# Kernel tuning notes

Hardware: AMD Instinct MI355X
Metric: run time of the kernel (lower is better)

The kernel has to match this reference:

```python
import jax, jax.numpy as jnp
import numpy as np

BN_EPS = 1e-5
NUM_GRAPHS = 64


def setup_inputs() -> dict:
    key = jax.random.key(0)
    ks = jax.random.split(key, 16)
    N, E, C_in, H, L, G = 100000, 1600000, 32, 64, 4, NUM_GRAPHS
    x = jax.random.normal(ks[0], (N, C_in), dtype=jnp.float32)
    edge_index = jax.random.randint(ks[1], (2, E), 0, N, dtype=jnp.int64)
    batch = jnp.sort(jax.random.randint(ks[2], (N,), 0, G, dtype=jnp.int64))
    s_in = 1.0 / np.sqrt(C_in)
    s_h = 1.0 / np.sqrt(H)
    s_2h = 1.0 / np.sqrt(2 * H)
    Win = jax.random.uniform(ks[3], (C_in, H), jnp.float32, -s_in, s_in)
    bin_ = jax.random.uniform(ks[4], (H,), jnp.float32, -s_in, s_in)
    W1s = jax.random.uniform(ks[5], (L, H, 2 * H), jnp.float32, -s_h, s_h)
    b1s = jax.random.uniform(ks[6], (L, 2 * H), jnp.float32, -s_h, s_h)
    gammas = jnp.ones((L, 2 * H), jnp.float32)
    betas = jnp.zeros((L, 2 * H), jnp.float32)
    W2s = jax.random.uniform(ks[7], (L, 2 * H, H), jnp.float32, -s_2h, s_2h)
    b2s = jax.random.uniform(ks[8], (L, H), jnp.float32, -s_2h, s_2h)
    epss = jnp.zeros((L,), jnp.float32)
    Wout = jax.random.uniform(ks[9], (H, 1), jnp.float32, -s_h, s_h)
    bout = jax.random.uniform(ks[10], (1,), jnp.float32, -s_h, s_h)
    return {"x": x, "edge_index": edge_index, "batch": batch, "Win": Win,
            "bin_": bin_, "W1s": W1s, "b1s": b1s, "gammas": gammas,
            "betas": betas, "W2s": W2s, "b2s": b2s, "epss": epss,
            "Wout": Wout, "bout": bout}


def _gin_layer(x, src, dst, W1, b1, gamma, beta, W2, b2, eps, n_nodes):
    # message: relu of source node features; aggregate: scatter-add at target
    agg = jax.ops.segment_sum(jax.nn.relu(x[src]), dst, num_segments=n_nodes)
    h = (1.0 + eps) * x + agg
    h = h @ W1 + b1
    mu = jnp.mean(h, axis=0)
    var = jnp.mean(jnp.square(h - mu), axis=0)  # biased, as in BatchNorm1d
    h = (h - mu) * jax.lax.rsqrt(var + BN_EPS) * gamma + beta
    h = jax.nn.relu(h)
    return h @ W2 + b2


def reference(x, edge_index, batch, Win, bin_, W1s, b1s, gammas, betas,
              W2s, b2s, epss, Wout, bout):
    N = x.shape[0]
    src, dst = edge_index[0], edge_index[1]
    x = x @ Win + bin_
    for l in range(W1s.shape[0]):
        x = x + _gin_layer(x, src, dst, W1s[l], b1s[l], gammas[l], betas[l],
                           W2s[l], b2s[l], epss[l], N)
    pooled = jax.ops.segment_sum(x, batch, num_segments=NUM_GRAPHS)  # [G, H]
    out = pooled @ Wout + bout
    return out.reshape(-1)
```

## Files before the change

kernel.cpp:

```cpp
#include <hip/hip_runtime.h>
#include <hip/hip_fp16.h>

#define H 64
#define CIN 32
#define TWOH 128
#define NGRAPH 64

#define BSH 7
#define BNODE 128
#define NBLK_PART 256
#define BCAP 32
#define MAXNB 2048
#define OCAP 65536

typedef unsigned short bfraw;
typedef _Float16 v8h __attribute__((ext_vector_type(8)));
typedef unsigned short v8u __attribute__((ext_vector_type(8)));
typedef float v4f __attribute__((ext_vector_type(4)));

union h8cast { v8u u; v8h h; uint4 q; };

__device__ __forceinline__ bfraw f2h(float f) {
    return __half_as_ushort(__float2half(f));
}
__device__ __forceinline__ float h2f(bfraw u) {
    return __half2float(__ushort_as_half(u));
}
__device__ __forceinline__ __half2 u2h2(unsigned u) {
    union { unsigned u; __half2 h; } c; c.u = u; return c.h;
}
__device__ __forceinline__ void f2h2(float f, _Float16& hi, _Float16& lo) {
    hi = (_Float16)f;
    lo = (_Float16)(f - (float)hi);
}

extern "C" __global__ void __launch_bounds__(256) k_input_gemm(
    const float* __restrict__ x, const float* __restrict__ Win,
    const float* __restrict__ bin, float* __restrict__ x0,
    bfraw* __restrict__ xh, int N)
{
    const int lane = threadIdx.x & 63;
    const int row = lane & 15;
    const int kg  = lane >> 4;
    v8h bhi[4], blo[4];
    #pragma unroll
    for (int ct = 0; ct < 4; ++ct) {
        v8h bh, bl;
        #pragma unroll
        for (int i = 0; i < 8; ++i) {
            const float w = Win[(kg * 8 + i) * H + ct * 16 + row];
            _Float16 h, l; f2h2(w, h, l);
            bh[i] = h; bl[i] = l;
        }
        bhi[ct] = bh; blo[ct] = bl;
    }
    float bcol[4];
    #pragma unroll
    for (int ct = 0; ct < 4; ++ct) bcol[ct] = bin[ct * 16 + row];

    const int wpb = blockDim.x >> 6;
    const int wid = blockIdx.x * wpb + (threadIdx.x >> 6);
    const int wstride = gridDim.x * wpb;
    const int tiles = (N + 15) >> 4;
    for (int t = wid; t < tiles; t += wstride) {
        const int tb = t << 4;
        int nA = tb + row; if (nA >= N) nA = N - 1;
        v8h a;
        #pragma unroll
        for (int i = 0; i < 8; ++i)
            a[i] = (_Float16)x[(size_t)nA * CIN + kg * 8 + i];
        v4f c[4];
        #pragma unroll
        for (int ct = 0; ct < 4; ++ct) {
            v4f cc = (v4f){0.f, 0.f, 0.f, 0.f};
            cc = __builtin_amdgcn_mfma_f32_16x16x32_f16(a, bhi[ct], cc, 0, 0, 0);
            cc = __builtin_amdgcn_mfma_f32_16x16x32_f16(a, blo[ct], cc, 0, 0, 0);
            c[ct] = cc;
        }
        #pragma unroll
        for (int ct = 0; ct < 4; ++ct) {
            #pragma unroll
            for (int r = 0; r < 4; ++r) {
                const int node = tb + kg * 4 + r;
                if (node < N) {
                    const float v = c[ct][r] + bcol[ct];
                    const size_t idx = (size_t)node * H + ct * 16 + row;
                    x0[idx] = v;
                    xh[idx] = f2h(fmaxf(v, 0.f));
                }
            }
        }
    }
}

extern "C" __global__ void k_cvtw(const float* __restrict__ W1s,
    const float* __restrict__ W2s, bfraw* __restrict__ W1hi,
    bfraw* __restrict__ W1lo, bfraw* __restrict__ W2hi,
    bfraw* __restrict__ W2lo, int total)
{
    int i = blockIdx.x * blockDim.x + threadIdx.x;
    const int st = gridDim.x * blockDim.x;
    for (; i < total; i += st) {
        {
            const float w = W1s[i];
            const bfraw hb = f2h(w);
            W1hi[i] = hb;
            W1lo[i] = f2h(w - h2f(hb));
        }
        {
            const float w = W2s[i];
            const bfraw hb = f2h(w);
            W2hi[i] = hb;
            W2lo[i] = f2h(w - h2f(hb));
        }
    }
}

__device__ __forceinline__ void bput(int s, int d, unsigned* __restrict__ lcnt,
    unsigned* __restrict__ myTmp, unsigned* __restrict__ deg,
    int* __restrict__ oflow, unsigned* __restrict__ ocnt)
{
    const int b = d >> BSH;
    const unsigned pos = atomicAdd(&lcnt[b], 1u);
    if (pos < BCAP) {
        myTmp[b * BCAP + pos] = (unsigned)s | ((unsigned)(d & (BNODE - 1)) << 20);
    } else {
        const unsigned o = atomicAdd(ocnt, 1u);
        if (o < OCAP) {
            oflow[2 * o] = s; oflow[2 * o + 1] = d;
            atomicAdd(&deg[d], 1u);
        }
    }
}

extern "C" __global__ void __launch_bounds__(256) k_bucket(
    const int* __restrict__ src, const int* __restrict__ dst,
    unsigned* __restrict__ bcnt, unsigned* __restrict__ btmp,
    unsigned* __restrict__ deg, int* __restrict__ oflow,
    unsigned* __restrict__ ocnt, int E, int NBck)
{
    __shared__ unsigned lcnt[MAXNB];
    for (int i = threadIdx.x; i < NBck; i += blockDim.x) lcnt[i] = 0u;
    __syncthreads();
    unsigned* __restrict__ myTmp = btmp + (size_t)blockIdx.x * NBck * BCAP;
    const int tid0 = blockIdx.x * blockDim.x + threadIdx.x;
    const int st = gridDim.x * blockDim.x;
    const int E4 = E >> 2;
    const int4* s4 = (const int4*)src;
    const int4* d4 = (const int4*)dst;
    for (int j = tid0; j < E4; j += st) {
        const int4 sv = s4[j];
        const int4 dv = d4[j];
        bput(sv.x, dv.x, lcnt, myTmp, deg, oflow, ocnt);
        bput(sv.y, dv.y, lcnt, myTmp, deg, oflow, ocnt);
        bput(sv.z, dv.z, lcnt, myTmp, deg, oflow, ocnt);
        bput(sv.w, dv.w, lcnt, myTmp, deg, oflow, ocnt);
    }
    for (int j = (E4 << 2) + tid0; j < E; j += st)
        bput(src[j], dst[j], lcnt, myTmp, deg, oflow, ocnt);
    __syncthreads();
    unsigned* __restrict__ myCnt = bcnt + (size_t)blockIdx.x * NBck;
    for (int i = threadIdx.x; i < NBck; i += blockDim.x) {
        const unsigned c = lcnt[i];
        myCnt[i] = (c < BCAP) ? c : BCAP;
    }
}

extern "C" __global__ void __launch_bounds__(256) k_bhist(
    const unsigned* __restrict__ bcnt, const unsigned* __restrict__ btmp,
    unsigned* __restrict__ deg, int N, int NBck)
{
    __shared__ unsigned hist[BNODE];
    const int b = blockIdx.x;
    for (int i = threadIdx.x; i < BNODE; i += blockDim.x) hist[i] = 0u;
    __syncthreads();
    for (int blk = threadIdx.x; blk < NBLK_PART; blk += blockDim.x) {
        const unsigned cnt = bcnt[(size_t)blk * NBck + b];
        const unsigned* p = btmp + ((size_t)blk * NBck + b) * BCAP;
        for (unsigned j = 0; j < cnt; ++j)
            atomicAdd(&hist[p[j] >> 20], 1u);
    }
    __syncthreads();
    const int base = b << BSH;
    for (int i = threadIdx.x; i < BNODE; i += blockDim.x)
        if (base + i < N) {
            const unsigned h = hist[i];
            if (h) atomicAdd(&deg[base + i], h);
        }
}

extern "C" __global__ void k_scan1(const unsigned* __restrict__ deg,
    unsigned* __restrict__ indptr, unsigned* __restrict__ bsum, int N)
{
    __shared__ unsigned s[256];
    const int tid = threadIdx.x;
    const int base = blockIdx.x * 1024 + tid * 4;
    unsigned d[4];
    #pragma unroll
    for (int j = 0; j < 4; ++j)
        d[j] = (base + j < N) ? ((deg[base + j] + 7u) & ~7u) : 0u;
    unsigned t = d[0] + d[1] + d[2] + d[3];
    s[tid] = t;
    __syncthreads();
    for (int o = 1; o < 256; o <<= 1) {
        unsigned v = (tid >= o) ? s[tid - o] : 0u;
        __syncthreads();
        s[tid] += v;
        __syncthreads();
    }
    unsigned run = (tid == 0) ? 0u : s[tid - 1];
    if (tid == 255) bsum[blockIdx.x] = s[255];
    #pragma unroll
    for (int j = 0; j < 4; ++j) {
        if (base + j < N) indptr[base + j] = run;
        run += d[j];
    }
}

extern "C" __global__ void k_scan2(unsigned* bsum, int nb,
    unsigned* __restrict__ indptr, int N,
    const float* __restrict__ bout, float* __restrict__ out)
{
    if (threadIdx.x < NGRAPH) out[threadIdx.x] = bout[0];
    if (threadIdx.x == 0) {
        unsigned run = 0;
        for (int i = 0; i < nb; ++i) { unsigned v = bsum[i]; bsum[i] = run; run += v; }
        indptr[N] = run;
    }
}

extern "C" __global__ void k_scan3(unsigned* __restrict__ indptr,
    const unsigned* __restrict__ bsum, unsigned* __restrict__ cursor, int N)
{
    const int base = blockIdx.x * 1024 + threadIdx.x * 4;
    const unsigned boff = bsum[blockIdx.x];
    #pragma unroll
    for (int j = 0; j < 4; ++j) {
        const int idx = base + j;
        if (idx < N) {
            const unsigned v = indptr[idx] + boff;
            indptr[idx] = v;
            cursor[idx] = v;
        }
    }
}

extern "C" __global__ void __launch_bounds__(256) k_bscat(
    const unsigned* __restrict__ bcnt, const unsigned* __restrict__ btmp,
    const unsigned* __restrict__ indptr, unsigned* __restrict__ cursor,
    int* __restrict__ esrc, int N, int NBck)
{
    __shared__ unsigned lcur[BNODE];
    const int b = blockIdx.x;
    const int base = b << BSH;
    for (int i = threadIdx.x; i < BNODE; i += blockDim.x)
        lcur[i] = (base + i < N) ? indptr[base + i] : 0u;
    __syncthreads();
    for (int blk = threadIdx.x; blk < NBLK_PART; blk += blockDim.x) {
        const unsigned cnt = bcnt[(size_t)blk * NBck + b];
        const unsigned* p = btmp + ((size_t)blk * NBck + b) * BCAP;
        for (unsigned j = 0; j < cnt; ++j) {
            const unsigned e = p[j];
            const unsigned pos = atomicAdd(&lcur[e >> 20], 1u);
            esrc[pos] = (int)(e & 0xFFFFFu);
        }
    }
    __syncthreads();
    for (int i = threadIdx.x; i < BNODE; i += blockDim.x)
        if (base + i < N) cursor[base + i] = lcur[i];
}

extern "C" __global__ void k_over(const int* __restrict__ oflow,
    const unsigned* __restrict__ ocnt, unsigned* __restrict__ cursor,
    int* __restrict__ esrc)
{
    unsigned n = *ocnt; if (n > OCAP) n = OCAP;
    int i = blockIdx.x * blockDim.x + threadIdx.x;
    const int st = gridDim.x * blockDim.x;
    for (; (unsigned)i < n; i += st) {
        const int s = oflow[2 * i], d = oflow[2 * i + 1];
        const unsigned pos = atomicAdd(&cursor[d], 1u);
        esrc[pos] = s;
    }
}

extern "C" __global__ void k_pad(const unsigned* __restrict__ cursor,
    const unsigned* __restrict__ indptr, int* __restrict__ esrc, int N)
{
    int n = blockIdx.x * blockDim.x + threadIdx.x;
    const int st = gridDim.x * blockDim.x;
    for (; n < N; n += st) {
        const unsigned end = indptr[n + 1];
        for (unsigned p = cursor[n]; p < end; ++p) esrc[p] = N;
    }
}

extern "C" __global__ void __launch_bounds__(256) k_agg(
    const float* __restrict__ x0, const bfraw* __restrict__ xh,
    const int* __restrict__ esrc, const unsigned* __restrict__ indptr,
    const float* __restrict__ epsp, bfraw* __restrict__ hpreh, int N)
{
    const int lane = threadIdx.x & 63;
    const int sub = lane >> 4;
    const int fi = (lane & 15) << 2;
    const int wpb = blockDim.x >> 6;
    int w = blockIdx.x * wpb + (threadIdx.x >> 6);
    const int wstride = gridDim.x * wpb;
    const float ep = 1.f + epsp[0];
    for (int n = w; n < N; n += wstride) {
        const unsigned s0 = indptr[n];
        const unsigned s1 = indptr[n + 1];
        float a0 = 0.f, a1 = 0.f, a2 = 0.f, a3 = 0.f;
        unsigned e = s0;
        for (; e + 16 <= s1; e += 16) {
            int idx[4];
            #pragma unroll
            for (int j = 0; j < 4; ++j) idx[j] = esrc[e + 4 * j + sub];
            uint2 r[4];
            #pragma unroll
            for (int j = 0; j < 4; ++j)
                r[j] = *(const uint2*)&xh[(size_t)idx[j] * H + fi];
            const __half2 s01 = __hadd2(__hadd2(u2h2(r[0].x), u2h2(r[1].x)),
                                        __hadd2(u2h2(r[2].x), u2h2(r[3].x)));
            const __half2 s23 = __hadd2(__hadd2(u2h2(r[0].y), u2h2(r[1].y)),
                                        __hadd2(u2h2(r[2].y), u2h2(r[3].y)));
            const float2 f01 = __half22float2(s01);
            const float2 f23 = __half22float2(s23);
            a0 += f01.x; a1 += f01.y; a2 += f23.x; a3 += f23.y;
        }
        for (; e + 8 <= s1; e += 8) {
            const int i0 = esrc[e + sub];
            const int i1 = esrc[e + 4 + sub];
            const uint2 r0 = *(const uint2*)&xh[(size_t)i0 * H + fi];
            const uint2 r1 = *(const uint2*)&xh[(size_t)i1 * H + fi];
            const float2 f01 = __half22float2(__hadd2(u2h2(r0.x), u2h2(r1.x)));
            const float2 f23 = __half22float2(__hadd2(u2h2(r0.y), u2h2(r1.y)));
            a0 += f01.x; a1 += f01.y; a2 += f23.x; a3 += f23.y;
        }
        for (; e < s1; e += 4) {
            const int i0 = esrc[e + sub];
            const uint2 r = *(const uint2*)&xh[(size_t)i0 * H + fi];
            const float2 f01 = __half22float2(u2h2(r.x));
            const float2 f23 = __half22float2(u2h2(r.y));
            a0 += f01.x; a1 += f01.y; a2 += f23.x; a3 += f23.y;
        }
        #pragma unroll
        for (int o = 16; o < 64; o <<= 1) {
            a0 += __shfl_xor(a0, o);
            a1 += __shfl_xor(a1, o);
            a2 += __shfl_xor(a2, o);
            a3 += __shfl_xor(a3, o);
        }
        if (sub == 0) {
            const float4 self = *(const float4*)&x0[(size_t)n * H + fi];
            ushort4 o;
            o.x = f2h(ep * self.x + a0);
            o.y = f2h(ep * self.y + a1);
            o.z = f2h(ep * self.z + a2);
            o.w = f2h(ep * self.w + a3);
            *(ushort4*)&hpreh[(size_t)n * H + fi] = o;
        }
    }
}

extern "C" __global__ void __launch_bounds__(256) k_gemm1(
    const bfraw* __restrict__ hpreh,
    const bfraw* __restrict__ W1hi, const bfraw* __restrict__ W1lo,
    const float* __restrict__ b1, bfraw* __restrict__ h1h,
    double* __restrict__ gsum, double* __restrict__ gsq, int N)
{
    __shared__ float ss[TWOH], sq[TWOH];
    if (threadIdx.x < TWOH) { ss[threadIdx.x] = 0.f; sq[threadIdx.x] = 0.f; }
    __syncthreads();
    const int lane = threadIdx.x & 63;
    const int row = lane & 15;
    const int kg  = lane >> 4;
    const int wpb = blockDim.x >> 6;
    const int wid = blockIdx.x * wpb + (threadIdx.x >> 6);
    const int wstride = gridDim.x * wpb;
    const int half = wid & 1;
    const int cb = half * 4;
    v8h bhi[2][4], blo[2][4];
    #pragma unroll
    for (int kc = 0; kc < 2; ++kc)
        #pragma unroll
        for (int ct = 0; ct < 4; ++ct) {
            v8h bh, bl;
            #pragma unroll
            for (int i = 0; i < 8; ++i) {
                const int idx = (kc * 32 + kg * 8 + i) * TWOH + (cb + ct) * 16 + row;
                bh[i] = (_Float16)__ushort_as_half(W1hi[idx]);
                bl[i] = (_Float16)__ushort_as_half(W1lo[idx]);
            }
            bhi[kc][ct] = bh; blo[kc][ct] = bl;
        }
    float bcol[4];
    #pragma unroll
    for (int ct = 0; ct < 4; ++ct) bcol[ct] = b1[(cb + ct) * 16 + row];

    const int tiles = (N + 15) >> 4;
    const int tstride = wstride >> 1;
    float sacc[4], qacc[4];
    #pragma unroll
    for (int ct = 0; ct < 4; ++ct) { sacc[ct] = 0.f; qacc[ct] = 0.f; }

    for (int t = wid >> 1; t < tiles; t += tstride) {
        const int tb = t << 4;
        int nA = tb + row; if (nA >= N) nA = N - 1;
        h8cast a0c, a1c;
        a0c.q = *(const uint4*)&hpreh[(size_t)nA * H + kg * 8];
        a1c.q = *(const uint4*)&hpreh[(size_t)nA * H + 32 + kg * 8];
        const v8h a0 = a0c.h;
        const v8h a1 = a1c.h;
        v4f c[4];
        #pragma unroll
        for (int ct = 0; ct < 4; ++ct) {
            v4f cc = (v4f){0.f, 0.f, 0.f, 0.f};
            cc = __builtin_amdgcn_mfma_f32_16x16x32_f16(a0, bhi[0][ct], cc, 0, 0, 0);
            cc = __builtin_amdgcn_mfma_f32_16x16x32_f16(a1, bhi[1][ct], cc, 0, 0, 0);
            cc = __builtin_amdgcn_mfma_f32_16x16x32_f16(a0, blo[0][ct], cc, 0, 0, 0);
            cc = __builtin_amdgcn_mfma_f32_16x16x32_f16(a1, blo[1][ct], cc, 0, 0, 0);
            c[ct] = cc;
        }
        #pragma unroll
        for (int ct = 0; ct < 4; ++ct) {
            #pragma unroll
            for (int r = 0; r < 4; ++r) {
                const int node = tb + kg * 4 + r;
                if (node < N) {
                    const float v = c[ct][r] + bcol[ct];
                    h1h[(size_t)node * TWOH + (cb + ct) * 16 + row] = f2h(v);
                    sacc[ct] += v;
                    qacc[ct] += v * v;
                }
            }
        }
    }
    #pragma unroll
    for (int ct = 0; ct < 4; ++ct) {
        float s = sacc[ct];
        s += __shfl_xor(s, 16); s += __shfl_xor(s, 32);
        float q = qacc[ct];
        q += __shfl_xor(q, 16); q += __shfl_xor(q, 32);
        if (kg == 0) {
            atomicAdd(&ss[(cb + ct) * 16 + row], s);
            atomicAdd(&sq[(cb + ct) * 16 + row], q);
        }
    }
    __syncthreads();
    if (threadIdx.x < TWOH) {
        atomicAdd(&gsum[threadIdx.x], (double)ss[threadIdx.x]);
        atomicAdd(&gsq[threadIdx.x], (double)sq[threadIdx.x]);
    }
}

extern "C" __global__ void __launch_bounds__(256) k_gemm2(
    const bfraw* __restrict__ h1h,
    const double* __restrict__ gsum, const double* __restrict__ gsq,
    const float* __restrict__ gamma, const float* __restrict__ beta,
    const bfraw* __restrict__ W2hi, const bfraw* __restrict__ W2lo,
    const float* __restrict__ b2, float* __restrict__ x0,
    bfraw* __restrict__ xh, int N)
{
    __shared__ float scl[TWOH], shl[TWOH];
    if (threadIdx.x < TWOH) {
        const int j = threadIdx.x;
        const double mu = gsum[j] / N;
        const double var = gsq[j] / N - mu * mu;
        const float sc = gamma[j] * rsqrtf(fmaxf((float)var, 0.f) + 1e-5f);
        scl[j] = sc;
        shl[j] = beta[j] - (float)mu * sc;
    }
    __syncthreads();
    const int lane = threadIdx.x & 63;
    const int row = lane & 15;
    const int kg  = lane >> 4;
    const int wpb = blockDim.x >> 6;
    const int wid = blockIdx.x * wpb + (threadIdx.x >> 6);
    const int wstride = gridDim.x * wpb;
    const int half = wid & 1;
    const int cb = half * 2;
    v8h bhi[4][2], blo[4][2];
    #pragma unroll
    for (int kc = 0; kc < 4; ++kc)
        #pragma unroll
        for (int ct = 0; ct < 2; ++ct) {
            v8h bh, bl;
            #pragma unroll
            for (int i = 0; i < 8; ++i) {
                const int idx = (kc * 32 + kg * 8 + i) * H + (cb + ct) * 16 + row;
                bh[i] = (_Float16)__ushort_as_half(W2hi[idx]);
                bl[i] = (_Float16)__ushort_as_half(W2lo[idx]);
            }
            bhi[kc][ct] = bh; blo[kc][ct] = bl;
        }
    float bcol[2];
    #pragma unroll
    for (int ct = 0; ct < 2; ++ct) bcol[ct] = b2[(cb + ct) * 16 + row];
    float lsc[4][8], lsh[4][8];
    #pragma unroll
    for (int kc = 0; kc < 4; ++kc) {
        const int fb = kc * 32 + kg * 8;
        #pragma unroll
        for (int i = 0; i < 8; ++i) { lsc[kc][i] = scl[fb + i]; lsh[kc][i] = shl[fb + i]; }
    }

    const int tiles = (N + 15) >> 4;
    const int tstride = wstride >> 1;

    for (int t = wid >> 1; t < tiles; t += tstride) {
        const int tb = t << 4;
        int nA = tb + row; if (nA >= N) nA = N - 1;
        v8h a[4];
        #pragma unroll
        for (int kc = 0; kc < 4; ++kc) {
            const int fb = kc * 32 + kg * 8;
            h8cast hc;
            hc.q = *(const uint4*)&h1h[(size_t)nA * TWOH + fb];
            v8h va;
            #pragma unroll
            for (int i = 0; i < 8; ++i) {
                const float hv = (float)hc.h[i];
                va[i] = (_Float16)fmaxf(hv * lsc[kc][i] + lsh[kc][i], 0.f);
            }
            a[kc] = va;
        }
        v4f c[2];
        #pragma unroll
        for (int ct = 0; ct < 2; ++ct) {
            v4f cc = (v4f){0.f, 0.f, 0.f, 0.f};
            #pragma unroll
            for (int kc = 0; kc < 4; ++kc) {
                cc = __builtin_amdgcn_mfma_f32_16x16x32_f16(a[kc], bhi[kc][ct], cc, 0, 0, 0);
                cc = __builtin_amdgcn_mfma_f32_16x16x32_f16(a[kc], blo[kc][ct], cc, 0, 0, 0);
            }
            c[ct] = cc;
        }
        #pragma unroll
        for (int ct = 0; ct < 2; ++ct) {
            #pragma unroll
            for (int r = 0; r < 4; ++r) {
                const int node = tb + kg * 4 + r;
                if (node < N) {
                    const size_t idx = (size_t)node * H + (cb + ct) * 16 + row;
                    const float v = x0[idx] + c[ct][r] + bcol[ct];
                    x0[idx] = v;
                    xh[idx] = f2h(fmaxf(v, 0.f));
                }
            }
        }
    }
}

extern "C" __global__ void __launch_bounds__(256) k_pool(
    const float* __restrict__ x0, const int* __restrict__ batch,
    const float* __restrict__ Wout, float* __restrict__ out, int N)
{
    const int lane = threadIdx.x & 63;
    const int wpb = blockDim.x >> 6;
    const int gw = blockIdx.x * wpb + (threadIdx.x >> 6);
    const int nw = gridDim.x * wpb;
    const int per = (N + nw - 1) / nw;
    const int n0 = gw * per;
    int n1 = n0 + per; if (n1 > N) n1 = N;
    if (n0 >= N) return;
    const float wv = Wout[lane];
    int cur = batch[n0];
    float acc = 0.f;
    for (int n = n0; n < n1; ++n) {
        const int g = batch[n];
        if (g != cur) {
            float v = acc * wv;
            #pragma unroll
            for (int o = 32; o > 0; o >>= 1) v += __shfl_down(v, o);
            if (lane == 0) atomicAdd(&out[cur], v);
            cur = g;
            acc = 0.f;
        }
        acc += x0[(size_t)n * H + lane];
    }
    float v = acc * wv;
    #pragma unroll
    for (int o = 32; o > 0; o >>= 1) v += __shfl_down(v, o);
    if (lane == 0) atomicAdd(&out[cur], v);
}

extern "C" void kernel_launch(void* const* d_in, const int* in_sizes, int n_in,
                              void* d_out, int out_size, void* d_ws, size_t ws_size,
                              hipStream_t stream)
{
    const float* x     = (const float*)d_in[0];
    const int*   ei    = (const int*)d_in[1];
    const int*   batch = (const int*)d_in[2];
    const float* Win   = (const float*)d_in[3];
    const float* bin   = (const float*)d_in[4];
    const float* W1s   = (const float*)d_in[5];
    const float* b1s   = (const float*)d_in[6];
    const float* gam   = (const float*)d_in[7];
    const float* bet   = (const float*)d_in[8];
    const float* W2s   = (const float*)d_in[9];
    const float* b2s   = (const float*)d_in[10];
    const float* epss  = (const float*)d_in[11];
    const float* Wout  = (const float*)d_in[12];
    const float* bout  = (const float*)d_in[13];

    const int N = in_sizes[0] / CIN;
    const int E = in_sizes[1] / 2;
    const int L = in_sizes[11];
    const int* src = ei;
    const int* dst = ei + E;
    const int NB = (N + BNODE - 1) >> BSH;

    char* ws = (char*)d_ws;
    size_t off = 0;
    auto take = [&](size_t bytes) {
        void* p = ws + off;
        off += (bytes + 255) & ~(size_t)255;
        return p;
    };
    float*    x0     = (float*)take((size_t)N * H * 4);
    bfraw*    xh     = (bfraw*)take((size_t)(N + 1) * H * 2);
    bfraw*    hpreh  = (bfraw*)take((size_t)N * H * 2);
    bfraw*    h1h    = (bfraw*)take((size_t)N * TWOH * 2);
    unsigned* deg    = (unsigned*)take((size_t)N * 4);
    unsigned* indptr = (unsigned*)take((size_t)(N + 1) * 4);
    unsigned* cursor = (unsigned*)take((size_t)N * 4);
    int*      esrc   = (int*)take((size_t)(E + 8 * (N + 1)) * 4);
    unsigned* bsum   = (unsigned*)take(4096);
    double*   gsumAll = (double*)take((size_t)8 * TWOH * 8 * 2);
    float*    scsh   = (float*)take(2 * TWOH * 4);
    bfraw*    W1hi   = (bfraw*)take((size_t)L * H * TWOH * 2);
    bfraw*    W1lo   = (bfraw*)take((size_t)L * H * TWOH * 2);
    bfraw*    W2hi   = (bfraw*)take((size_t)L * TWOH * H * 2);
    bfraw*    W2lo   = (bfraw*)take((size_t)L * TWOH * H * 2);
    unsigned* bcnt   = (unsigned*)take((size_t)NBLK_PART * NB * 4);
    unsigned* btmp   = (unsigned*)take((size_t)NBLK_PART * NB * BCAP * 4);
    int*      oflow  = (int*)take((size_t)OCAP * 2 * 4);
    unsigned* ocnt   = (unsigned*)take(256);
    (void)ws_size; (void)n_in; (void)out_size; (void)scsh;

    hipMemsetAsync(deg, 0, (size_t)N * 4, stream);
    hipMemsetAsync(ocnt, 0, 4, stream);
    hipMemsetAsync(xh + (size_t)N * H, 0, H * 2, stream);
    hipMemsetAsync(gsumAll, 0, (size_t)8 * TWOH * 8 * 2, stream);
    k_input_gemm<<<512, 256, 0, stream>>>(x, Win, bin, x0, xh, N);
    k_cvtw<<<256, 256, 0, stream>>>(W1s, W2s, W1hi, W1lo, W2hi, W2lo, L * H * TWOH);
    k_bucket<<<NBLK_PART, 256, 0, stream>>>(src, dst, bcnt, btmp, deg, oflow, ocnt, E, NB);
    k_bhist<<<NB, 256, 0, stream>>>(bcnt, btmp, deg, N, NB);
    const int nb = (N + 1023) / 1024;
    k_scan1<<<nb, 256, 0, stream>>>(deg, indptr, bsum, N);
    k_scan2<<<1, 64, 0, stream>>>(bsum, nb, indptr, N, bout, (float*)d_out);
    k_scan3<<<nb, 256, 0, stream>>>(indptr, bsum, cursor, N);
    k_bscat<<<NB, 256, 0, stream>>>(bcnt, btmp, indptr, cursor, esrc, N, NB);
    k_over<<<32, 256, 0, stream>>>(oflow, ocnt, cursor, esrc);
    k_pad<<<512, 256, 0, stream>>>(cursor, indptr, esrc, N);

    for (int l = 0; l < L; ++l) {
        double* gsum = gsumAll + (size_t)l * 2 * TWOH;
        double* gsq  = gsum + TWOH;
        k_agg<<<4096, 256, 0, stream>>>(x0, xh, esrc, indptr, epss + l, hpreh, N);
        k_gemm1<<<512, 256, 0, stream>>>(hpreh,
            W1hi + (size_t)l * H * TWOH, W1lo + (size_t)l * H * TWOH,
            b1s + (size_t)l * TWOH, h1h, gsum, gsq, N);
        k_gemm2<<<512, 256, 0, stream>>>(h1h, gsum, gsq,
            gam + (size_t)l * TWOH, bet + (size_t)l * TWOH,
            W2hi + (size_t)l * TWOH * H, W2lo + (size_t)l * TWOH * H,
            b2s + (size_t)l * H, x0, xh, N);
    }

    k_pool<<<512, 256, 0, stream>>>(x0, batch, Wout, (float*)d_out, N);
}
```

Measured before the change: 456.5 us.

## Assign one node per 16-lane group in aggregation instead of one per wavefront

The aggregation kernel now has each 16-lane quarter-wave own a separate node and loop over its whole edge list in padded 8-edge chunks. Indices are read with vector int4 loads, and the cross-group shuffle reduction is gone. The grid is halved to match the four-nodes-per-wave mapping. This relies on the padding to multiples of 8 being aligned for the int4 loads, and nodes within a wave with different degrees now cause divergence.

Result: no change. 448.1 us, median of 2 (-1.8%).

```diff
diff --git a/kernel.cpp b/kernel.cpp
--- a/kernel.cpp
+++ b/kernel.cpp
@@ -301,57 +301,44 @@
     const float* __restrict__ epsp, bfraw* __restrict__ hpreh, int N)
 {
     const int lane = threadIdx.x & 63;
-    const int sub = lane >> 4;
+    const int grp = lane >> 4;
     const int fi = (lane & 15) << 2;
     const int wpb = blockDim.x >> 6;
-    int w = blockIdx.x * wpb + (threadIdx.x >> 6);
+    const int wid = blockIdx.x * wpb + (threadIdx.x >> 6);
     const int wstride = gridDim.x * wpb;
     const float ep = 1.f + epsp[0];
-    for (int n = w; n < N; n += wstride) {
-        const unsigned s0 = indptr[n];
-        const unsigned s1 = indptr[n + 1];
+    for (int nb = wid << 2; nb < N; nb += wstride << 2) {
+        const int n = nb + grp;
+        const bool act = (n < N);
+        unsigned s0 = 0, s1 = 0;
+        if (act) { s0 = indptr[n]; s1 = indptr[n + 1]; }
         float a0 = 0.f, a1 = 0.f, a2 = 0.f, a3 = 0.f;
-        unsigned e = s0;
-        for (; e + 16 <= s1; e += 16) {
-            int idx[4];
-            #pragma unroll
-            for (int j = 0; j < 4; ++j) idx[j] = esrc[e + 4 * j + sub];
-            uint2 r[4];
-            #pragma unroll
-            for (int j = 0; j < 4; ++j)
-                r[j] = *(const uint2*)&xh[(size_t)idx[j] * H + fi];
-            const __half2 s01 = __hadd2(__hadd2(u2h2(r[0].x), u2h2(r[1].x)),
-                                        __hadd2(u2h2(r[2].x), u2h2(r[3].x)));
-            const __half2 s23 = __hadd2(__hadd2(u2h2(r[0].y), u2h2(r[1].y)),
-                                        __hadd2(u2h2(r[2].y), u2h2(r[3].y)));
+        for (unsigned e = s0; e < s1; e += 8) {
+            const int4 ia = *(const int4*)&esrc[e];
+            const int4 ib = *(const int4*)&esrc[e + 4];
+            uint2 r0 = *(const uint2*)&xh[(size_t)ia.x * H + fi];
+            uint2 r1 = *(const uint2*)&xh[(size_t)ia.y * H + fi];
+            uint2 r2 = *(const uint2*)&xh[(size_t)ia.z * H + fi];
+            uint2 r3 = *(const uint2*)&xh[(size_t)ia.w * H + fi];
+            uint2 r4 = *(const uint2*)&xh[(size_t)ib.x * H + fi];
+            uint2 r5 = *(const uint2*)&xh[(size_t)ib.y * H + fi];
+            uint2 r6 = *(const uint2*)&xh[(size_t)ib.z * H + fi];
+            uint2 r7 = *(const uint2*)&xh[(size_t)ib.w * H + fi];
+            const __half2 s01 =
+                __hadd2(__hadd2(__hadd2(u2h2(r0.x), u2h2(r1.x)),
+                                __hadd2(u2h2(r2.x), u2h2(r3.x))),
+                        __hadd2(__hadd2(u2h2(r4.x), u2h2(r5.x)),
+                                __hadd2(u2h2(r6.x), u2h2(r7.x))));
+            const __half2 s23 =
+                __hadd2(__hadd2(__hadd2(u2h2(r0.y), u2h2(r1.y)),
+                                __hadd2(u2h2(r2.y), u2h2(r3.y))),
+                        __hadd2(__hadd2(u2h2(r4.y), u2h2(r5.y)),
+                                __hadd2(u2h2(r6.y), u2h2(r7.y))));
             const float2 f01 = __half22float2(s01);
             const float2 f23 = __half22float2(s23);
             a0 += f01.x; a1 += f01.y; a2 += f23.x; a3 += f23.y;
         }
-        for (; e + 8 <= s1; e += 8) {
-            const int i0 = esrc[e + sub];
-            const int i1 = esrc[e + 4 + sub];
-            const uint2 r0 = *(const uint2*)&xh[(size_t)i0 * H + fi];
-            const uint2 r1 = *(const uint2*)&xh[(size_t)i1 * H + fi];
-            const float2 f01 = __half22float2(__hadd2(u2h2(r0.x), u2h2(r1.x)));
-            const float2 f23 = __half22float2(__hadd2(u2h2(r0.y), u2h2(r1.y)));
-            a0 += f01.x; a1 += f01.y; a2 += f23.x; a3 += f23.y;
-        }
-        for (; e < s1; e += 4) {
-            const int i0 = esrc[e + sub];
-            const uint2 r = *(const uint2*)&xh[(size_t)i0 * H + fi];
-            const float2 f01 = __half22float2(u2h2(r.x));
-            const float2 f23 = __half22float2(u2h2(r.y));
-            a0 += f01.x; a1 += f01.y; a2 += f23.x; a3 += f23.y;
-        }
-        #pragma unroll
-        for (int o = 16; o < 64; o <<= 1) {
-            a0 += __shfl_xor(a0, o);
-            a1 += __shfl_xor(a1, o);
-            a2 += __shfl_xor(a2, o);
-            a3 += __shfl_xor(a3, o);
-        }
-        if (sub == 0) {
+        if (act) {
             const float4 self = *(const float4*)&x0[(size_t)n * H + fi];
             ushort4 o;
             o.x = f2h(ep * self.x + a0);
@@ -628,7 +615,6 @@
     int*      esrc   = (int*)take((size_t)(E + 8 * (N + 1)) * 4);
     unsigned* bsum   = (unsigned*)take(4096);
     double*   gsumAll = (double*)take((size_t)8 * TWOH * 8 * 2);
-    float*    scsh   = (float*)take(2 * TWOH * 4);
     bfraw*    W1hi   = (bfraw*)take((size_t)L * H * TWOH * 2);
     bfraw*    W1lo   = (bfraw*)take((size_t)L * H * TWOH * 2);
     bfraw*    W2hi   = (bfraw*)take((size_t)L * TWOH * H * 2);
@@ -637,7 +623,7 @@
     unsigned* btmp   = (unsigned*)take((size_t)NBLK_PART * NB * BCAP * 4);
     int*      oflow  = (int*)take((size_t)OCAP * 2 * 4);
     unsigned* ocnt   = (unsigned*)take(256);
-    (void)ws_size; (void)n_in; (void)out_size; (void)scsh;
+    (void)ws_size; (void)n_in; (void)out_size;
 
     hipMemsetAsync(deg, 0, (size_t)N * 4, stream);
     hipMemsetAsync(ocnt, 0, 4, stream);
@@ -658,7 +644,7 @@
     for (int l = 0; l < L; ++l) {
         double* gsum = gsumAll + (size_t)l * 2 * TWOH;
         double* gsq  = gsum + TWOH;
-        k_agg<<<4096, 256, 0, stream>>>(x0, xh, esrc, indptr, epss + l, hpreh, N);
+        k_agg<<<2048, 256, 0, stream>>>(x0, xh, esrc, indptr, epss + l, hpreh, N);
         k_gemm1<<<512, 256, 0, stream>>>(hpreh,
             W1hi + (size_t)l * H * TWOH, W1lo + (size_t)l * H * TWOH,
             b1s + (size_t)l * TWOH, h1h, gsum, gsq, N);
```
